# Optimization experiments

Hardware: AMD Instinct MI355X
Metric: run time of the kernel (lower is better)

Reference implementation:

```python
import jax, jax.numpy as jnp
import numpy as np
from jax import lax

B, T, F_IN, H = 256, 800, 3, 200  # batch, time_steps, n_features, n_hidden=time_steps//4


def hard_sigmoid(z):
    return jnp.clip(0.2 * z + 0.5, 0.0, 1.0)


def lstm_hardsigmoid(x_btf, Wih, Whh, bih, bhh):
    """Unidirectional single-layer LSTM, hard-sigmoid gates, zero init state.
    x_btf: (B, T, F); Wih: (4H, F); Whh: (4H, H); biases: (4H,). Returns (B, T, H)."""
    Hh = Whh.shape[1]
    # input contribution for all timesteps at once: (B, T, 4H)
    pre = jnp.einsum('btf,gf->btg', x_btf, Wih) + bih + bhh
    pre_tb = jnp.swapaxes(pre, 0, 1)  # (T, B, 4H)
    b = x_btf.shape[0]
    init = (jnp.zeros((b, Hh), x_btf.dtype), jnp.zeros((b, Hh), x_btf.dtype))

    def step(carry, pre_t):
        h, c = carry
        gates = pre_t + h @ Whh.T  # (B, 4H)
        i, f, g, o = jnp.split(gates, 4, axis=-1)  # torch gate order i,f,g,o
        i = hard_sigmoid(i)
        f = hard_sigmoid(f)
        g = jnp.tanh(g)
        o = hard_sigmoid(o)
        c_new = f * c + i * g
        h_new = o * jnp.tanh(c_new)
        return (h_new, c_new), h_new

    _, hs = lax.scan(step, init, pre_tb)  # hs: (T, B, H)
    return jnp.swapaxes(hs, 0, 1)


def setup_inputs() -> dict:
    key = jax.random.key(0)
    ks = jax.random.split(key, 4)
    return {
        'x': jax.random.normal(ks[0], (B, F_IN, T), jnp.float32),
        'enc_Wih': jax.random.normal(ks[1], (4 * H, F_IN), jnp.float32) * 0.1,
        'enc_Whh': jax.random.normal(ks[2], (4 * H, H), jnp.float32) * 0.05,
        'enc_bih': jnp.zeros((4 * H,), jnp.float32),
        'enc_bhh': jnp.zeros((4 * H,), jnp.float32),
        'dec_Wih': jax.random.normal(ks[3], (4 * F_IN, H), jnp.float32) * 0.05,
        'dec_Whh': jax.random.normal(jax.random.fold_in(key, 7), (4 * F_IN, F_IN), jnp.float32) * 0.1,
        'dec_bih': jnp.zeros((4 * F_IN,), jnp.float32),
        'dec_bhh': jnp.zeros((4 * F_IN,), jnp.float32),
    }


def reference(x, enc_Wih, enc_Whh, enc_bih, enc_bhh, dec_Wih, dec_Whh, dec_bih, dec_bhh):
    # x: (B, n_features, T) -> permute -> (B, T, n_features)
    xi = jnp.transpose(x, (0, 2, 1))
    enc_out = lstm_hardsigmoid(xi, enc_Wih, enc_Whh, enc_bih, enc_bhh)  # (B, T, H)
    # max_pool1d over time (kernel = full length) == max over T
    pooled = jnp.max(enc_out, axis=1)  # (B, H)
    # repeat pooled vector for every timestep
    dec_in = jnp.broadcast_to(pooled[:, None, :], (pooled.shape[0], T, H))
    dec_out = lstm_hardsigmoid(dec_in, dec_Wih, dec_Whh, dec_bih, dec_bhh)  # (B, T, F)
    return jnp.transpose(dec_out, (0, 2, 1))  # (B, n_features, T)
```

## Files before the change

kernel.cpp:

```cpp
#include <hip/hip_runtime.h>
#include <hip/hip_fp16.h>
#include <stdint.h>


typedef _Float16 half2_t __attribute__((ext_vector_type(2)));

__device__ __forceinline__ float fdot2f(uint32_t hp, uint32_t wp, float acc) {
#if __has_builtin(__builtin_amdgcn_fdot2)
  return __builtin_amdgcn_fdot2(__builtin_bit_cast(half2_t, hp),
                                __builtin_bit_cast(half2_t, wp), acc, false);
#else
  half2_t a = __builtin_bit_cast(half2_t, hp);
  half2_t b = __builtin_bit_cast(half2_t, wp);
  return acc + (float)a[0] * (float)b[0] + (float)a[1] * (float)b[1];
#endif
}

__device__ __forceinline__ float hsig(float z) {
  return fminf(fmaxf(__builtin_fmaf(0.2f, z, 0.5f), 0.f), 1.f);
}

__device__ __forceinline__ float tanh_fast(float v) {
  float e = __builtin_amdgcn_exp2f(v * 2.885390081777927f);
  return 1.f - 2.f * __builtin_amdgcn_rcpf(e + 1.f);
}

__global__ void prep_kernel(const float* __restrict__ whh,
                            uint32_t* __restrict__ wpk) {
  int idx = blockIdx.x * 256 + threadIdx.x;
  if (idx >= 80000) return;
  int p = idx / 800;
  int j = idx - p * 800;
  float a = whh[j * 200 + 2 * p];
  float b = whh[j * 200 + 2 * p + 1];
  __half2 v = __floats2half2_rn(a, b);
  wpk[idx] = __builtin_bit_cast(uint32_t, v);
}

__global__ __launch_bounds__(448, 1)
void enc_kernel(const float* __restrict__ x,
                const float* __restrict__ wih,
                const float* __restrict__ bih,
                const float* __restrict__ bhh,
                const uint32_t* __restrict__ wpk,
                const float* __restrict__ dwih,
                const float* __restrict__ dbih,
                const float* __restrict__ dbhh,
                float* __restrict__ pre12)
{
  const int b = blockIdx.x;
  const int t = threadIdx.x;

  __shared__ float xs[3 * 800];
  __shared__ alignas(16) __half hh[200];
  __shared__ float gates[800];
  __shared__ float pooled[200];

  for (int i = t; i < 2400; i += 448) xs[i] = x[(size_t)b * 2400 + i];
  if (t < 200) hh[t] = __float2half(0.f);

  const bool worker = t < 400;
  uint32_t w1[100], w2[100];
  float bias1 = 0.f, bias2 = 0.f;
  float wiA0 = 0, wiA1 = 0, wiA2 = 0, wiB0 = 0, wiB1 = 0, wiB2 = 0;
  if (worker) {
    const int r1 = t, r2 = t + 400;
#pragma unroll
    for (int p = 0; p < 100; ++p) {
      w1[p] = wpk[p * 800 + r1];
      w2[p] = wpk[p * 800 + r2];
    }
    bias1 = bih[r1] + bhh[r1];
    bias2 = bih[r2] + bhh[r2];
    wiA0 = wih[r1 * 3 + 0]; wiA1 = wih[r1 * 3 + 1]; wiA2 = wih[r1 * 3 + 2];
    wiB0 = wih[r2 * 3 + 0]; wiB1 = wih[r2 * 3 + 1]; wiB2 = wih[r2 * 3 + 2];
  }
  float c_state = 0.f;
  float maxh = -INFINITY;
  __syncthreads();

  for (int step = 0; step < 800; ++step) {
    if (worker) {
      float a0 = 0.f, a1 = 0.f, d0 = 0.f, d1 = 0.f;
      const uint4* H4 = (const uint4*)hh;
#pragma unroll
      for (int q = 0; q < 25; ++q) {
        uint4 Hv = H4[q];
        a0 = fdot2f(Hv.x, w1[4 * q + 0], a0);
        d0 = fdot2f(Hv.x, w2[4 * q + 0], d0);
        a1 = fdot2f(Hv.y, w1[4 * q + 1], a1);
        d1 = fdot2f(Hv.y, w2[4 * q + 1], d1);
        a0 = fdot2f(Hv.z, w1[4 * q + 2], a0);
        d0 = fdot2f(Hv.z, w2[4 * q + 2], d0);
        a1 = fdot2f(Hv.w, w1[4 * q + 3], a1);
        d1 = fdot2f(Hv.w, w2[4 * q + 3], d1);
      }
      float x0 = xs[step], x1 = xs[800 + step], x2 = xs[1600 + step];
      float g1 = a0 + a1 + bias1;
      g1 = __builtin_fmaf(wiA0, x0, g1);
      g1 = __builtin_fmaf(wiA1, x1, g1);
      g1 = __builtin_fmaf(wiA2, x2, g1);
      float g2 = d0 + d1 + bias2;
      g2 = __builtin_fmaf(wiB0, x0, g2);
      g2 = __builtin_fmaf(wiB1, x1, g2);
      g2 = __builtin_fmaf(wiB2, x2, g2);
      gates[t] = g1;
      gates[t + 400] = g2;
    }
    __syncthreads();
    if (t < 200) {
      float gi = gates[t], gf = gates[t + 200], gg = gates[t + 400], go = gates[t + 600];
      float i_ = hsig(gi), f_ = hsig(gf), o_ = hsig(go);
      float g_ = tanh_fast(gg);
      c_state = f_ * c_state + i_ * g_;
      float h_ = o_ * tanh_fast(c_state);
      maxh = fmaxf(maxh, h_);
      hh[t] = __float2half(h_);
    }
    __syncthreads();
  }

  if (t < 200) pooled[t] = maxh;
  __syncthreads();
  if (t < 12) {
    float s = dbih[t] + dbhh[t];
    const float* wr = dwih + t * 200;
#pragma unroll 8
    for (int u = 0; u < 200; ++u) s = __builtin_fmaf(pooled[u], wr[u], s);
    pre12[b * 12 + t] = s;
  }
}

__global__ __launch_bounds__(64, 1)
void dec_kernel(const float* __restrict__ pre12,
                const float* __restrict__ dwhh,
                float* __restrict__ out)
{
  const int lane = threadIdx.x;
  const int b = blockIdx.x * 64 + lane;

  float pre[12];
#pragma unroll
  for (int j = 0; j < 12; ++j) pre[j] = pre12[b * 12 + j];
  float W[36];
#pragma unroll
  for (int j = 0; j < 36; ++j) W[j] = dwhh[j];

  float h0 = 0, h1 = 0, h2 = 0, c0 = 0, c1 = 0, c2 = 0;
  int tc = 800;
  float* ob = out + (size_t)b * 2400;

  for (int step = 0; step < 800; ++step) {
    float g[12];
#pragma unroll
    for (int j = 0; j < 12; ++j) {
      float v = pre[j];
      v = __builtin_fmaf(W[j * 3 + 0], h0, v);
      v = __builtin_fmaf(W[j * 3 + 1], h1, v);
      v = __builtin_fmaf(W[j * 3 + 2], h2, v);
      g[j] = v;
    }
    float nc0 = hsig(g[3]) * c0 + hsig(g[0]) * tanh_fast(g[6]);
    float nc1 = hsig(g[4]) * c1 + hsig(g[1]) * tanh_fast(g[7]);
    float nc2 = hsig(g[5]) * c2 + hsig(g[2]) * tanh_fast(g[8]);
    float nh0 = hsig(g[9])  * tanh_fast(nc0);
    float nh1 = hsig(g[10]) * tanh_fast(nc1);
    float nh2 = hsig(g[11]) * tanh_fast(nc2);
    bool same = (nh0 == h0) && (nh1 == h1) && (nh2 == h2) &&
                (nc0 == c0) && (nc1 == c1) && (nc2 == c2);
    ob[step] = nh0; ob[800 + step] = nh1; ob[1600 + step] = nh2;
    h0 = nh0; h1 = nh1; h2 = nh2; c0 = nc0; c1 = nc1; c2 = nc2;
    if (same) { tc = step + 1; break; }
  }

  __shared__ int s_tc[64];
  __shared__ float s_h[64][3];
  s_tc[lane] = tc;
  s_h[lane][0] = h0; s_h[lane][1] = h1; s_h[lane][2] = h2;
  __syncthreads();
  for (int i = 0; i < 64; ++i) {
    const int start = s_tc[i];
    if (start >= 800) continue;
    float v0 = s_h[i][0], v1 = s_h[i][1], v2 = s_h[i][2];
    float* op = out + (size_t)(blockIdx.x * 64 + i) * 2400;
    for (int tt = start + lane; tt < 800; tt += 64) {
      op[tt] = v0; op[800 + tt] = v1; op[1600 + tt] = v2;
    }
  }
}

extern "C" void kernel_launch(void* const* d_in, const int* in_sizes, int n_in,
                              void* d_out, int out_size, void* d_ws, size_t ws_size,
                              hipStream_t stream)
{
  const float* x    = (const float*)d_in[0];
  const float* wih  = (const float*)d_in[1];
  const float* whh  = (const float*)d_in[2];
  const float* bih  = (const float*)d_in[3];
  const float* bhh  = (const float*)d_in[4];
  const float* dwih = (const float*)d_in[5];
  const float* dwhh = (const float*)d_in[6];
  const float* dbih = (const float*)d_in[7];
  const float* dbhh = (const float*)d_in[8];
  float* out = (float*)d_out;

  uint32_t* wpk = (uint32_t*)d_ws;
  float* pre12  = (float*)((char*)d_ws + 320000);

  hipLaunchKernelGGL(prep_kernel, dim3(313), dim3(256), 0, stream, whh, wpk);
  hipLaunchKernelGGL(enc_kernel, dim3(256), dim3(448), 0, stream,
                     x, wih, bih, bhh, wpk, dwih, dbih, dbhh, pre12);
  hipLaunchKernelGGL(dec_kernel, dim3(4), dim3(64), 0, stream, pre12, dwhh, out);
}
```

Measured before the change: 1.187 ms.

## Fuse decoder into encoder kernel and use one gate row per thread

The encoder block grows from 448 to 832 threads so each of 800 worker threads owns one gate row, not two, and applies its activation before writing to shared memory. This halves the per-thread dot-product chain on the serial recurrence path and leaves 200 threads doing only the cell update. The separate decoder kernel is removed: each encoder block runs its own batch element's decoder in three lanes, stores the history in shared memory, then writes the output with 800 threads, filling steps after early convergence from the last value. The trade-off is heavier register and occupancy pressure from the larger block, plus a serial decoder tail inside every block.

```diff
diff --git a/kernel.cpp b/kernel.cpp
--- a/kernel.cpp
+++ b/kernel.cpp
@@ -37,7 +37,7 @@
   wpk[idx] = __builtin_bit_cast(uint32_t, v);
 }
 
-__global__ __launch_bounds__(448, 1)
+__global__ __launch_bounds__(832, 1)
 void enc_kernel(const float* __restrict__ x,
                 const float* __restrict__ wih,
                 const float* __restrict__ bih,
@@ -46,34 +46,31 @@
                 const float* __restrict__ dwih,
                 const float* __restrict__ dbih,
                 const float* __restrict__ dbhh,
-                float* __restrict__ pre12)
+                const float* __restrict__ dwhh,
+                float* __restrict__ out)
 {
   const int b = blockIdx.x;
   const int t = threadIdx.x;
 
-  __shared__ float xs[3 * 800];
+  __shared__ float xs[2400];
   __shared__ alignas(16) __half hh[200];
   __shared__ float gates[800];
   __shared__ float pooled[200];
+  __shared__ float pre12s[12];
+  __shared__ int s_tc;
 
-  for (int i = t; i < 2400; i += 448) xs[i] = x[(size_t)b * 2400 + i];
+  for (int i = t; i < 2400; i += 832) xs[i] = x[(size_t)b * 2400 + i];
   if (t < 200) hh[t] = __float2half(0.f);
 
-  const bool worker = t < 400;
-  uint32_t w1[100], w2[100];
-  float bias1 = 0.f, bias2 = 0.f;
-  float wiA0 = 0, wiA1 = 0, wiA2 = 0, wiB0 = 0, wiB1 = 0, wiB2 = 0;
+  const bool worker = t < 800;
+  const int gtype = t / 200;
+  uint32_t w[100];
+  float bias = 0.f, wi0 = 0.f, wi1 = 0.f, wi2 = 0.f;
   if (worker) {
-    const int r1 = t, r2 = t + 400;
 #pragma unroll
-    for (int p = 0; p < 100; ++p) {
-      w1[p] = wpk[p * 800 + r1];
-      w2[p] = wpk[p * 800 + r2];
-    }
-    bias1 = bih[r1] + bhh[r1];
-    bias2 = bih[r2] + bhh[r2];
-    wiA0 = wih[r1 * 3 + 0]; wiA1 = wih[r1 * 3 + 1]; wiA2 = wih[r1 * 3 + 2];
-    wiB0 = wih[r2 * 3 + 0]; wiB1 = wih[r2 * 3 + 1]; wiB2 = wih[r2 * 3 + 2];
+    for (int p = 0; p < 100; ++p) w[p] = wpk[p * 800 + t];
+    bias = bih[t] + bhh[t];
+    wi0 = wih[t * 3 + 0]; wi1 = wih[t * 3 + 1]; wi2 = wih[t * 3 + 2];
   }
   float c_state = 0.f;
   float maxh = -INFINITY;
@@ -81,39 +78,30 @@
 
   for (int step = 0; step < 800; ++step) {
     if (worker) {
-      float a0 = 0.f, a1 = 0.f, d0 = 0.f, d1 = 0.f;
+      float a0 = 0.f, a1 = 0.f;
       const uint4* H4 = (const uint4*)hh;
 #pragma unroll
       for (int q = 0; q < 25; ++q) {
         uint4 Hv = H4[q];
-        a0 = fdot2f(Hv.x, w1[4 * q + 0], a0);
-        d0 = fdot2f(Hv.x, w2[4 * q + 0], d0);
-        a1 = fdot2f(Hv.y, w1[4 * q + 1], a1);
-        d1 = fdot2f(Hv.y, w2[4 * q + 1], d1);
-        a0 = fdot2f(Hv.z, w1[4 * q + 2], a0);
-        d0 = fdot2f(Hv.z, w2[4 * q + 2], d0);
-        a1 = fdot2f(Hv.w, w1[4 * q + 3], a1);
-        d1 = fdot2f(Hv.w, w2[4 * q + 3], d1);
+        a0 = fdot2f(Hv.x, w[4 * q + 0], a0);
+        a1 = fdot2f(Hv.y, w[4 * q + 1], a1);
+        a0 = fdot2f(Hv.z, w[4 * q + 2], a0);
+        a1 = fdot2f(Hv.w, w[4 * q + 3], a1);
       }
-      float x0 = xs[step], x1 = xs[800 + step], x2 = xs[1600 + step];
-      float g1 = a0 + a1 + bias1;
-      g1 = __builtin_fmaf(wiA0, x0, g1);
-      g1 = __builtin_fmaf(wiA1, x1, g1);
-      g1 = __builtin_fmaf(wiA2, x2, g1);
-      float g2 = d0 + d1 + bias2;
-      g2 = __builtin_fmaf(wiB0, x0, g2);
-      g2 = __builtin_fmaf(wiB1, x1, g2);
-      g2 = __builtin_fmaf(wiB2, x2, g2);
-      gates[t] = g1;
-      gates[t + 400] = g2;
+      float g = a0 + a1 + bias;
+      g = __builtin_fmaf(wi0, xs[step], g);
+      g = __builtin_fmaf(wi1, xs[800 + step], g);
+      g = __builtin_fmaf(wi2, xs[1600 + step], g);
+      float act;
+      if (gtype == 2) act = tanh_fast(g); else act = hsig(g);
+      gates[t] = act;
     }
     __syncthreads();
     if (t < 200) {
-      float gi = gates[t], gf = gates[t + 200], gg = gates[t + 400], go = gates[t + 600];
-      float i_ = hsig(gi), f_ = hsig(gf), o_ = hsig(go);
-      float g_ = tanh_fast(gg);
-      c_state = f_ * c_state + i_ * g_;
-      float h_ = o_ * tanh_fast(c_state);
+      float ai = gates[t], af = gates[t + 200];
+      float ag = gates[t + 400], ao = gates[t + 600];
+      c_state = __builtin_fmaf(af, c_state, ai * ag);
+      float h_ = ao * tanh_fast(c_state);
       maxh = fmaxf(maxh, h_);
       hh[t] = __float2half(h_);
     }
@@ -127,64 +115,56 @@
     const float* wr = dwih + t * 200;
 #pragma unroll 8
     for (int u = 0; u < 200; ++u) s = __builtin_fmaf(pooled[u], wr[u], s);
-    pre12[b * 12 + t] = s;
+    pre12s[t] = s;
   }
-}
+  __syncthreads();
 
-__global__ __launch_bounds__(64, 1)
-void dec_kernel(const float* __restrict__ pre12,
-                const float* __restrict__ dwhh,
-                float* __restrict__ out)
-{
-  const int lane = threadIdx.x;
-  const int b = blockIdx.x * 64 + lane;
+  if (t < 3) {
+    float pre[12];
+#pragma unroll
+    for (int j = 0; j < 12; ++j) pre[j] = pre12s[j];
+    float W[36];
+#pragma unroll
+    for (int j = 0; j < 36; ++j) W[j] = dwhh[j];
 
-  float pre[12];
+    float h0 = 0, h1 = 0, h2 = 0, c0 = 0, c1 = 0, c2 = 0;
+    int tc = 800;
+    float* hist = xs + t * 800;
+    for (int step = 0; step < 800; ++step) {
+      float g[12];
 #pragma unroll
-  for (int j = 0; j < 12; ++j) pre[j] = pre12[b * 12 + j];
-  float W[36];
-#pragma unroll
-  for (int j = 0; j < 36; ++j) W[j] = dwhh[j];
+      for (int j = 0; j < 12; ++j) {
+        float v = pre[j];
+        v = __builtin_fmaf(W[j * 3 + 0], h0, v);
+        v = __builtin_fmaf(W[j * 3 + 1], h1, v);
+        v = __builtin_fmaf(W[j * 3 + 2], h2, v);
+        g[j] = v;
+      }
+      float nc0 = hsig(g[3]) * c0 + hsig(g[0]) * tanh_fast(g[6]);
+      float nc1 = hsig(g[4]) * c1 + hsig(g[1]) * tanh_fast(g[7]);
+      float nc2 = hsig(g[5]) * c2 + hsig(g[2]) * tanh_fast(g[8]);
+      float nh0 = hsig(g[9])  * tanh_fast(nc0);
+      float nh1 = hsig(g[10]) * tanh_fast(nc1);
+      float nh2 = hsig(g[11]) * tanh_fast(nc2);
+      bool same = (nh0 == h0) && (nh1 == h1) && (nh2 == h2) &&
+                  (nc0 == c0) && (nc1 == c1) && (nc2 == c2);
+      float mine = (t == 0) ? nh0 : ((t == 1) ? nh1 : nh2);
+      hist[step] = mine;
+      h0 = nh0; h1 = nh1; h2 = nh2; c0 = nc0; c1 = nc1; c2 = nc2;
+      if (same) { tc = step + 1; break; }
+    }
+    if (t == 0) s_tc = tc;
+  }
+  __syncthreads();
 
-  float h0 = 0, h1 = 0, h2 = 0, c0 = 0, c1 = 0, c2 = 0;
-  int tc = 800;
-  float* ob = out + (size_t)b * 2400;
-
-  for (int step = 0; step < 800; ++step) {
-    float g[12];
-#pragma unroll
-    for (int j = 0; j < 12; ++j) {
-      float v = pre[j];
-      v = __builtin_fmaf(W[j * 3 + 0], h0, v);
-      v = __builtin_fmaf(W[j * 3 + 1], h1, v);
-      v = __builtin_fmaf(W[j * 3 + 2], h2, v);
-      g[j] = v;
-    }
-    float nc0 = hsig(g[3]) * c0 + hsig(g[0]) * tanh_fast(g[6]);
-    float nc1 = hsig(g[4]) * c1 + hsig(g[1]) * tanh_fast(g[7]);
-    float nc2 = hsig(g[5]) * c2 + hsig(g[2]) * tanh_fast(g[8]);
-    float nh0 = hsig(g[9])  * tanh_fast(nc0);
-    float nh1 = hsig(g[10]) * tanh_fast(nc1);
-    float nh2 = hsig(g[11]) * tanh_fast(nc2);
-    bool same = (nh0 == h0) && (nh1 == h1) && (nh2 == h2) &&
-                (nc0 == c0) && (nc1 == c1) && (nc2 == c2);
-    ob[step] = nh0; ob[800 + step] = nh1; ob[1600 + step] = nh2;
-    h0 = nh0; h1 = nh1; h2 = nh2; c0 = nc0; c1 = nc1; c2 = nc2;
-    if (same) { tc = step + 1; break; }
-  }
-
-  __shared__ int s_tc[64];
-  __shared__ float s_h[64][3];
-  s_tc[lane] = tc;
-  s_h[lane][0] = h0; s_h[lane][1] = h1; s_h[lane][2] = h2;
-  __syncthreads();
-  for (int i = 0; i < 64; ++i) {
-    const int start = s_tc[i];
-    if (start >= 800) continue;
-    float v0 = s_h[i][0], v1 = s_h[i][1], v2 = s_h[i][2];
-    float* op = out + (size_t)(blockIdx.x * 64 + i) * 2400;
-    for (int tt = start + lane; tt < 800; tt += 64) {
-      op[tt] = v0; op[800 + tt] = v1; op[1600 + tt] = v2;
+  {
+    const int tc1 = s_tc - 1;
+    float* ob = out + (size_t)b * 2400;
+    if (t < 800) {
+      int idx = (t < s_tc) ? t : tc1;
+      ob[t]        = xs[idx];
+      ob[800 + t]  = xs[800 + idx];
+      ob[1600 + t] = xs[1600 + idx];
     }
   }
 }
@@ -205,10 +185,8 @@
   float* out = (float*)d_out;
 
   uint32_t* wpk = (uint32_t*)d_ws;
-  float* pre12  = (float*)((char*)d_ws + 320000);
 
   hipLaunchKernelGGL(prep_kernel, dim3(313), dim3(256), 0, stream, whh, wpk);
-  hipLaunchKernelGGL(enc_kernel, dim3(256), dim3(448), 0, stream,
-                     x, wih, bih, bhh, wpk, dwih, dbih, dbhh, pre12);
-  hipLaunchKernelGGL(dec_kernel, dim3(4), dim3(64), 0, stream, pre12, dwhh, out);
+  hipLaunchKernelGGL(enc_kernel, dim3(256), dim3(832), 0, stream,
+                     x, wih, bih, bhh, wpk, dwih, dbih, dbhh, dwhh, out);
 }
```

Result: no change. 1.205 ms (+1.5%).

## Batch 16 sequences per block and run encoder recurrence on MFMA

Applied to the files above, without the earlier changes.

The encoder moves from one block per sequence using fdot2 dot products to one block per 16 sequences, computing the recurrent matmul with 16x16x32 f16 MFMA instructions. Weights are prepacked into MFMA fragment layout, with the input projection and bias folded in as extra K columns fed by x and a constant 1. Gate rows are interleaved so each lane's accumulator holds i,f,g,o for one hidden unit, which removes the separate gates shared-memory pass and one barrier per step. Hidden state is double-buffered in LDS and the fragments are pinned in AGPRs. The trade-off is only 16 blocks on the GPU, so parallelism drops sharply, and each step now runs 13 serial MFMA tiles per wave.

```diff
diff --git a/kernel.cpp b/kernel.cpp
--- a/kernel.cpp
+++ b/kernel.cpp
@@ -3,131 +3,158 @@
 #include <stdint.h>
 
 
-typedef _Float16 half2_t __attribute__((ext_vector_type(2)));
-
-__device__ __forceinline__ float fdot2f(uint32_t hp, uint32_t wp, float acc) {
-#if __has_builtin(__builtin_amdgcn_fdot2)
-  return __builtin_amdgcn_fdot2(__builtin_bit_cast(half2_t, hp),
-                                __builtin_bit_cast(half2_t, wp), acc, false);
-#else
-  half2_t a = __builtin_bit_cast(half2_t, hp);
-  half2_t b = __builtin_bit_cast(half2_t, wp);
-  return acc + (float)a[0] * (float)b[0] + (float)a[1] * (float)b[1];
-#endif
-}
+typedef _Float16 f16x8 __attribute__((ext_vector_type(8)));
+typedef float f32x4 __attribute__((ext_vector_type(4)));
+
+#define MT_TILES 52
+#define KT_TILES 7
+#define TPW 13
+#define HSTR 116
 
 __device__ __forceinline__ float hsig(float z) {
   return fminf(fmaxf(__builtin_fmaf(0.2f, z, 0.5f), 0.f), 1.f);
 }
-
 __device__ __forceinline__ float tanh_fast(float v) {
   float e = __builtin_amdgcn_exp2f(v * 2.885390081777927f);
   return 1.f - 2.f * __builtin_amdgcn_rcpf(e + 1.f);
 }
 
 __global__ void prep_kernel(const float* __restrict__ whh,
-                            uint32_t* __restrict__ wpk) {
+                            const float* __restrict__ wih,
+                            const float* __restrict__ bih,
+                            const float* __restrict__ bhh,
+                            uint32_t* __restrict__ wpkA) {
   int idx = blockIdx.x * 256 + threadIdx.x;
-  if (idx >= 80000) return;
-  int p = idx / 800;
-  int j = idx - p * 800;
-  float a = whh[j * 200 + 2 * p];
-  float b = whh[j * 200 + 2 * p + 1];
-  __half2 v = __floats2half2_rn(a, b);
-  wpk[idx] = __builtin_bit_cast(uint32_t, v);
-}
-
-__global__ __launch_bounds__(448, 1)
+  if (idx >= MT_TILES * KT_TILES * 256) return;
+  int v = idx & 3;
+  int l = (idx >> 2) & 63;
+  int mk = idx >> 8;
+  int kt = mk % KT_TILES, mta = mk / KT_TILES;
+  int rl = l & 15;
+  int u = mta * 4 + (rl >> 2);
+  int g = rl & 3;
+  int kb = kt * 32 + (l >> 4) * 8 + 2 * v;
+  float e0 = 0.f, e1 = 0.f;
+  if (u < 200) {
+    int orig = u + 200 * g;
+    int k0 = kb, k1 = kb + 1;
+    e0 = (k0 < 200) ? whh[orig * 200 + k0]
+       : (k0 < 203) ? wih[orig * 3 + (k0 - 200)]
+       : (k0 == 203) ? (bih[orig] + bhh[orig]) : 0.f;
+    e1 = (k1 < 200) ? whh[orig * 200 + k1]
+       : (k1 < 203) ? wih[orig * 3 + (k1 - 200)]
+       : (k1 == 203) ? (bih[orig] + bhh[orig]) : 0.f;
+  }
+  __half2 h = __floats2half2_rn(e0, e1);
+  wpkA[idx] = __builtin_bit_cast(uint32_t, h);
+}
+
+__global__ __launch_bounds__(256, 1)
 void enc_kernel(const float* __restrict__ x,
-                const float* __restrict__ wih,
-                const float* __restrict__ bih,
-                const float* __restrict__ bhh,
-                const uint32_t* __restrict__ wpk,
+                const uint32_t* __restrict__ wpkA,
                 const float* __restrict__ dwih,
                 const float* __restrict__ dbih,
                 const float* __restrict__ dbhh,
-                float* __restrict__ pre12)
+                float* __restrict__ pre12g)
 {
-  const int b = blockIdx.x;
+  const int bt = blockIdx.x;
   const int t = threadIdx.x;
-
-  __shared__ float xs[3 * 800];
-  __shared__ alignas(16) __half hh[200];
-  __shared__ float gates[800];
-  __shared__ float pooled[200];
-
-  for (int i = t; i < 2400; i += 448) xs[i] = x[(size_t)b * 2400 + i];
-  if (t < 200) hh[t] = __float2half(0.f);
-
-  const bool worker = t < 400;
-  uint32_t w1[100], w2[100];
-  float bias1 = 0.f, bias2 = 0.f;
-  float wiA0 = 0, wiA1 = 0, wiA2 = 0, wiB0 = 0, wiB1 = 0, wiB2 = 0;
-  if (worker) {
-    const int r1 = t, r2 = t + 400;
-#pragma unroll
-    for (int p = 0; p < 100; ++p) {
-      w1[p] = wpk[p * 800 + r1];
-      w2[p] = wpk[p * 800 + r2];
+  const int lane = t & 63;
+  const int w = t >> 6;
+  const int col = lane & 15;
+  const int kq = lane >> 4;
+
+  __shared__ uint32_t hbuf[2][16 * HSTR];
+  __shared__ float pooled[16][200];
+
+  for (int i = t; i < 2 * 16 * HSTR; i += 256) ((uint32_t*)hbuf)[i] = 0;
+
+  f16x8 wf[TPW][KT_TILES];
+#pragma unroll
+  for (int mt = 0; mt < TPW; ++mt)
+#pragma unroll
+    for (int kt = 0; kt < KT_TILES; ++kt) {
+      int mta = w * TPW + mt;
+      uint4 uv = ((const uint4*)wpkA)[(mta * KT_TILES + kt) * 64 + lane];
+      wf[mt][kt] = __builtin_bit_cast(f16x8, uv);
     }
-    bias1 = bih[r1] + bhh[r1];
-    bias2 = bih[r2] + bhh[r2];
-    wiA0 = wih[r1 * 3 + 0]; wiA1 = wih[r1 * 3 + 1]; wiA2 = wih[r1 * 3 + 2];
-    wiB0 = wih[r2 * 3 + 0]; wiB1 = wih[r2 * 3 + 1]; wiB2 = wih[r2 * 3 + 2];
-  }
-  float c_state = 0.f;
-  float maxh = -INFINITY;
-  __syncthreads();
-
-  for (int step = 0; step < 800; ++step) {
-    if (worker) {
-      float a0 = 0.f, a1 = 0.f, d0 = 0.f, d1 = 0.f;
-      const uint4* H4 = (const uint4*)hh;
-#pragma unroll
-      for (int q = 0; q < 25; ++q) {
-        uint4 Hv = H4[q];
-        a0 = fdot2f(Hv.x, w1[4 * q + 0], a0);
-        d0 = fdot2f(Hv.x, w2[4 * q + 0], d0);
-        a1 = fdot2f(Hv.y, w1[4 * q + 1], a1);
-        d1 = fdot2f(Hv.y, w2[4 * q + 1], d1);
-        a0 = fdot2f(Hv.z, w1[4 * q + 2], a0);
-        d0 = fdot2f(Hv.z, w2[4 * q + 2], d0);
-        a1 = fdot2f(Hv.w, w1[4 * q + 3], a1);
-        d1 = fdot2f(Hv.w, w2[4 * q + 3], d1);
-      }
-      float x0 = xs[step], x1 = xs[800 + step], x2 = xs[1600 + step];
-      float g1 = a0 + a1 + bias1;
-      g1 = __builtin_fmaf(wiA0, x0, g1);
-      g1 = __builtin_fmaf(wiA1, x1, g1);
-      g1 = __builtin_fmaf(wiA2, x2, g1);
-      float g2 = d0 + d1 + bias2;
-      g2 = __builtin_fmaf(wiB0, x0, g2);
-      g2 = __builtin_fmaf(wiB1, x1, g2);
-      g2 = __builtin_fmaf(wiB2, x2, g2);
-      gates[t] = g1;
-      gates[t + 400] = g2;
-    }
-    __syncthreads();
-    if (t < 200) {
-      float gi = gates[t], gf = gates[t + 200], gg = gates[t + 400], go = gates[t + 600];
-      float i_ = hsig(gi), f_ = hsig(gf), o_ = hsig(go);
-      float g_ = tanh_fast(gg);
-      c_state = f_ * c_state + i_ * g_;
-      float h_ = o_ * tanh_fast(c_state);
-      maxh = fmaxf(maxh, h_);
-      hh[t] = __float2half(h_);
-    }
-    __syncthreads();
-  }
-
-  if (t < 200) pooled[t] = maxh;
-  __syncthreads();
-  if (t < 12) {
-    float s = dbih[t] + dbhh[t];
-    const float* wr = dwih + t * 200;
+#pragma unroll
+  for (int mt = 0; mt < TPW; ++mt)
+#pragma unroll
+    for (int kt = 0; kt < KT_TILES; ++kt)
+      asm volatile("" : "+a"(wf[mt][kt]));
+
+  const float* xb = x + (size_t)(bt * 16 + col) * 2400;
+  __syncthreads();
+  if (w == 0 && lane < 16) {
+    __half2 p01 = __floats2half2_rn(xb[0], xb[800]);
+    __half2 p23 = __floats2half2_rn(xb[1600], 1.0f);
+    hbuf[0][col * HSTR + 100] = __builtin_bit_cast(uint32_t, p01);
+    hbuf[0][col * HSTR + 101] = __builtin_bit_cast(uint32_t, p23);
+  }
+  __syncthreads();
+
+  float cst[TPW], mx[TPW];
+#pragma unroll
+  for (int mt = 0; mt < TPW; ++mt) { cst[mt] = 0.f; mx[mt] = -INFINITY; }
+
+  const int rdoff = col * HSTR + kq * 4;
+
+#define ENC_STEP(SRC, DST, TT)                                               \
+  {                                                                          \
+    float x0 = 0.f, x1 = 0.f, x2 = 0.f;                                      \
+    const bool dox = (w == 0) && (lane < 16) && ((TT) < 799);                \
+    if (dox) { x0 = xb[(TT) + 1]; x1 = xb[800 + (TT) + 1];                   \
+               x2 = xb[1600 + (TT) + 1]; }                                   \
+    f16x8 bf[KT_TILES];                                                      \
+    _Pragma("unroll")                                                        \
+    for (int kt = 0; kt < KT_TILES; ++kt)                                    \
+      bf[kt] = __builtin_bit_cast(f16x8,                                     \
+                 *(const uint4*)&hbuf[SRC][rdoff + kt * 16]);                \
+    _Pragma("unroll")                                                        \
+    for (int mt = 0; mt < TPW; ++mt) {                                       \
+      f32x4 C = {0.f, 0.f, 0.f, 0.f};                                        \
+      _Pragma("unroll")                                                      \
+      for (int kt = 0; kt < KT_TILES; ++kt)                                  \
+        C = __builtin_amdgcn_mfma_f32_16x16x32_f16(wf[mt][kt], bf[kt], C,    \
+                                                   0, 0, 0);                 \
+      float i_ = hsig(C[0]), f_ = hsig(C[1]), o_ = hsig(C[3]);               \
+      float g_ = tanh_fast(C[2]);                                            \
+      cst[mt] = __builtin_fmaf(f_, cst[mt], i_ * g_);                        \
+      float h_ = o_ * tanh_fast(cst[mt]);                                    \
+      mx[mt] = fmaxf(mx[mt], h_);                                            \
+      int u = (w * TPW + mt) * 4 + kq;                                       \
+      if (u < 200)                                                           \
+        ((__half*)hbuf[DST])[col * 232 + u] = __float2half(h_);              \
+    }                                                                        \
+    if (dox) {                                                               \
+      __half2 p01 = __floats2half2_rn(x0, x1);                               \
+      __half2 p23 = __floats2half2_rn(x2, 1.0f);                             \
+      hbuf[DST][col * HSTR + 100] = __builtin_bit_cast(uint32_t, p01);       \
+      hbuf[DST][col * HSTR + 101] = __builtin_bit_cast(uint32_t, p23);       \
+    }                                                                        \
+    __syncthreads();                                                         \
+  }
+
+  for (int sp = 0; sp < 400; ++sp) {
+    ENC_STEP(0, 1, 2 * sp)
+    ENC_STEP(1, 0, 2 * sp + 1)
+  }
+#undef ENC_STEP
+
+#pragma unroll
+  for (int mt = 0; mt < TPW; ++mt) {
+    int u = (w * TPW + mt) * 4 + kq;
+    if (u < 200) pooled[col][u] = mx[mt];
+  }
+  __syncthreads();
+  if (t < 192) {
+    int b = t / 12, j = t % 12;
+    float s = dbih[j] + dbhh[j];
+    const float* wr = dwih + j * 200;
 #pragma unroll 8
-    for (int u = 0; u < 200; ++u) s = __builtin_fmaf(pooled[u], wr[u], s);
-    pre12[b * 12 + t] = s;
+    for (int u2 = 0; u2 < 200; ++u2) s = __builtin_fmaf(pooled[b][u2], wr[u2], s);
+    pre12g[(bt * 16 + b) * 12 + j] = s;
   }
 }
 
@@ -204,11 +231,13 @@
   const float* dbhh = (const float*)d_in[8];
   float* out = (float*)d_out;
 
-  uint32_t* wpk = (uint32_t*)d_ws;
-  float* pre12  = (float*)((char*)d_ws + 320000);
-
-  hipLaunchKernelGGL(prep_kernel, dim3(313), dim3(256), 0, stream, whh, wpk);
-  hipLaunchKernelGGL(enc_kernel, dim3(256), dim3(448), 0, stream,
-                     x, wih, bih, bhh, wpk, dwih, dbih, dbhh, pre12);
-  hipLaunchKernelGGL(dec_kernel, dim3(4), dim3(64), 0, stream, pre12, dwhh, out);
-}
+  uint32_t* wpkA = (uint32_t*)d_ws;
+  float* pre12g  = (float*)((char*)d_ws + 372736);
+
+  hipLaunchKernelGGL(prep_kernel, dim3(364), dim3(256), 0, stream,
+                     whh, wih, bih, bhh, wpkA);
+  hipLaunchKernelGGL(enc_kernel, dim3(16), dim3(256), 0, stream,
+                     x, wpkA, dwih, dbih, dbhh, pre12g);
+  hipLaunchKernelGGL(dec_kernel, dim3(4), dim3(64), 0, stream,
+                     pre12g, dwhh, out);
+}
```

Result: slower. 1.694 ms (+42.7%).
